# Kernel tuning notes

Measured on AMD Instinct MI355X. Metric: run time of the kernel, lower is better.

Reference implementation:

```python
import jax, jax.numpy as jnp
import numpy as np

DIM = 256
HEADS = 8
CAMS = 6
MINSIZE = 25  # AdaptiveAvgPool2d output size = min(feature_map_size)


def layernorm(x, g, b, eps=1e-5):
    mu = x.mean(-1, keepdims=True)
    var = ((x - mu) ** 2).mean(-1, keepdims=True)
    return (x - mu) / jnp.sqrt(var + eps) * g + b


def setup_inputs() -> dict:
    key = jax.random.key(0)
    ks = jax.random.split(key, 16)
    d, n = DIM, CAMS
    s = 0.02
    inp = {}
    inp["q"] = jax.random.normal(ks[0], (2, n, d, 50, 50), jnp.float32)
    inp["k"] = jax.random.normal(ks[1], (2, n, d, 50, 50), jnp.float32)
    inp["v"] = jax.random.normal(ks[2], (2, n, d, 50, 50), jnp.float32)
    inp["Wq"] = jax.random.normal(ks[3], (d, d), jnp.float32) * s
    inp["bq"] = jnp.zeros((d,), jnp.float32)
    inp["Wk"] = jax.random.normal(ks[4], (d, d), jnp.float32) * s
    inp["bk"] = jnp.zeros((d,), jnp.float32)
    inp["Wv"] = jax.random.normal(ks[5], (d, d), jnp.float32) * s
    inp["bv"] = jnp.zeros((d,), jnp.float32)
    inp["Wproj"] = jax.random.normal(ks[6], (n * d, d), jnp.float32) * s
    inp["bproj"] = jnp.zeros((d,), jnp.float32)
    inp["Waddq"] = jax.random.normal(ks[7], (n * d, d), jnp.float32) * s
    inp["baddq"] = jnp.zeros((d,), jnp.float32)
    inp["W1"] = jax.random.normal(ks[8], (d, 2 * d), jnp.float32) * s
    inp["b1"] = jnp.zeros((2 * d,), jnp.float32)
    inp["W2"] = jax.random.normal(ks[9], (2 * d, d), jnp.float32) * s
    inp["b2"] = jnp.zeros((d,), jnp.float32)
    inp["g_pre"] = jnp.ones((n * d,), jnp.float32)
    inp["b_pre"] = jnp.zeros((n * d,), jnp.float32)
    inp["g_norm"] = jnp.ones((d,), jnp.float32)
    inp["b_norm"] = jnp.zeros((d,), jnp.float32)
    return inp


def reference(q, k, v, Wq, bq, Wk, bk, Wv, bv, Wproj, bproj, Waddq, baddq,
              W1, b1, W2, b2, g_pre, b_pre, g_norm, b_norm):
    B, n, d, H, W = q.shape
    m = HEADS
    dh = d // m
    Q = H * W

    # residual query path: (b n d H W) -> (b HW (n d)) -> add_qproj -> (b HW d)
    add_q = jnp.transpose(q, (0, 3, 4, 1, 2)).reshape(B, Q, n * d) @ Waddq + baddq

    # queries: (b n d H W) -> (b n HW d) -> to_q
    qf = jnp.transpose(q, (0, 1, 3, 4, 2)).reshape(B, n, Q, d) @ Wq + bq

    # adaptive avg pool to MINSIZE (exact 2x2 bins since 50 = 2*25)
    def pool(t):
        _, _, _, h, w = t.shape
        return t.reshape(B, n, d, MINSIZE, h // MINSIZE, MINSIZE, w // MINSIZE).mean((4, 6))

    kp = pool(k)  # (b n d 25 25)
    vp = pool(v)
    K = MINSIZE * MINSIZE
    # (avg pool commutes with the pointwise linear to_k/to_v)
    kf = jnp.transpose(kp, (0, 1, 3, 4, 2)).reshape(B, n, K, d) @ Wk + bk
    vf = jnp.transpose(vp, (0, 1, 3, 4, 2)).reshape(B, n, K, d) @ Wv + bv

    # split heads
    qh = qf.reshape(B, n, Q, m, dh)
    kh = kf.reshape(B, n, K, m, dh)
    vh = vf.reshape(B, n, K, m, dh)

    # per-camera scores, softmax jointly over concatenated camera keys
    scores = (dh ** -0.5) * jnp.einsum('bnqmd,bnkmd->bmqnk', qh, kh)  # (B,m,Q,n,K)
    attn = jax.nn.softmax(scores.reshape(B, m, Q, n * K), axis=-1).reshape(B, m, Q, n, K)

    # per-camera attention output, concat cams (and heads within each cam) -> (B,Q,n*d)
    out = jnp.einsum('bmqnk,bnkmd->bqnmd', attn, vh).reshape(B, Q, n * d)

    x = layernorm(out, g_pre, b_pre) @ Wproj + bproj  # (B,Q,d)
    x = x + add_q
    h1 = jax.nn.gelu(x @ W1 + b1, approximate=False)
    x = x + layernorm(h1 @ W2 + b2, g_norm, b_norm)
    return jnp.transpose(x.reshape(B, H, W, d), (0, 3, 1, 2))  # (B,d,H,W)
```

## Files before the change

### kernel.cpp

```cpp
#include <hip/hip_runtime.h>
#include <math.h>

#define BATCH 2
#define NCAM 6
#define DIM 256
#define HEADS 8
#define DH 32
#define HW 2500
#define KP 625
#define NDIM (NCAM*DIM)

typedef __attribute__((ext_vector_type(8))) short short8;
typedef __attribute__((ext_vector_type(4))) float f32x4;

__device__ __forceinline__ short f2bf(float f) {
    union { float f; unsigned u; } v; v.f = f;
    unsigned r = v.u + 0x7fffu + ((v.u >> 16) & 1u);
    return (short)(r >> 16);
}
__device__ __forceinline__ float bf2f(short h) {
    union { unsigned u; float f; } v; v.u = ((unsigned)(unsigned short)h) << 16;
    return v.f;
}

struct WJ { const float* src; short* dst; int K, N; };
struct WArgs { WJ j[7]; };

__global__ __launch_bounds__(256) void prep_all(
    const float* __restrict__ q, const float* __restrict__ k,
    const float* __restrict__ v, short* __restrict__ qbf,
    short* __restrict__ kpbf, short* __restrict__ vpbf, WArgs wa)
{
    __shared__ float t[32][33];
    const int tx = threadIdx.x & 31, ty = threadIdx.x >> 5;
    int i = blockIdx.x;
    if (i < 7584) {
        int slab = i / 632, rem = i % 632;
        int hwB = (rem % 79) * 32, dB = (rem / 79) * 32;
        const float* src = q + (size_t)slab * 640000;
#pragma unroll
        for (int ii = 0; ii < 32; ii += 8) {
            int hw = hwB + tx;
            t[ty + ii][tx] = (hw < HW) ? src[(size_t)(dB + ty + ii) * HW + hw] : 0.f;
        }
        __syncthreads();
#pragma unroll
        for (int ii = 0; ii < 32; ii += 8) {
            int hw = hwB + ty + ii;
            if (hw < HW)
                qbf[((size_t)slab * HW + hw) * DIM + dB + tx] = f2bf(t[tx][ty + ii]);
        }
    } else if (i < 11424) {
        int i2 = i - 7584;
        const float* base; short* dst;
        if (i2 < 1920) { base = k; dst = kpbf; }
        else           { base = v; dst = vpbf; i2 -= 1920; }
        int slab = i2 / 160, rem = i2 % 160;
        int kpB = (rem % 20) * 32, dB = (rem / 20) * 32;
        const float* src = base + (size_t)slab * 640000;
        dst += (size_t)slab * (KP * DIM);
#pragma unroll
        for (int ii = 0; ii < 32; ii += 8) {
            int kp = kpB + tx;
            float val = 0.f;
            if (kp < KP) {
                int r2 = (kp / 25) * 2, c2 = (kp % 25) * 2;
                const float* p0 = src + (size_t)(dB + ty + ii) * HW + r2 * 50 + c2;
                val = 0.25f * (p0[0] + p0[1] + p0[50] + p0[51]);
            }
            t[ty + ii][tx] = val;
        }
        __syncthreads();
#pragma unroll
        for (int ii = 0; ii < 32; ii += 8) {
            int kp = kpB + ty + ii;
            if (kp < KP)
                dst[(size_t)kp * DIM + dB + tx] = f2bf(t[tx][ty + ii]);
        }
    } else {
        int wi = i - 11424;
        WJ jb = wa.j[0];
        for (int jj = 0; jj < 7; jj++) {
            jb = wa.j[jj];
            int cnt = (jb.K >> 5) * (jb.N >> 5);
            if (wi < cnt) break;
            wi -= cnt;
        }
        int tn = jb.N >> 5;
        int nB = (wi % tn) * 32, kB = (wi / tn) * 32;
#pragma unroll
        for (int ii = 0; ii < 32; ii += 8)
            t[ty + ii][tx] = jb.src[(size_t)(kB + ty + ii) * jb.N + nB + tx];
        __syncthreads();
#pragma unroll
        for (int ii = 0; ii < 32; ii += 8)
            jb.dst[(size_t)(nB + ty + ii) * jb.K + kB + tx] = f2bf(t[tx][ty + ii]);
    }
}

struct GJob { const short* A; const short* Bt; const float* bias;
              short* Cb; float* Cf; int M, K, yb, mode; };
struct GArgs { GJob j[4]; };

__global__ __launch_bounds__(256) void gemm_in(GArgs ga) {
    GJob jb = ga.j[blockIdx.z];
    if ((int)blockIdx.y >= jb.yb) return;
    __shared__ short As[64 * 32];
    __shared__ short Bs[64 * 32];

    const int tid  = threadIdx.x;
    const int nB   = blockIdx.x * 64;
    const int rB   = blockIdx.y * 64;
    const int w    = tid >> 6;
    const int lane = tid & 63;
    const int l15  = lane & 15;
    const int quad = lane >> 4;
    const int M = jb.M, K = jb.K;

    f32x4 acc[4];
#pragma unroll
    for (int jt = 0; jt < 4; jt++) acc[jt] = (f32x4){0.f, 0.f, 0.f, 0.f};

    const int r = tid >> 2, gk = tid & 3;
    const int rg = rB + r;
    const int bb = rg / 2500, hwp = rg % 2500;

    for (int kB = 0; kB < K; kB += 32) {
        __syncthreads();
        short8 a0 = {0, 0, 0, 0, 0, 0, 0, 0};
        if (rg < M) {
            if (jb.mode) {
                int kk = kB + gk * 8;
                int cam = kk >> 8, c = kk & 255;
                a0 = *(const short8*)&jb.A[(((size_t)(bb * 6 + cam)) * HW + hwp) * DIM + c];
            } else {
                a0 = *(const short8*)&jb.A[(size_t)rg * K + kB + gk * 8];
            }
        }
        *(short8*)&As[r * 32 + ((gk ^ (r & 3)) << 3)] = a0;
        short8 bv = *(const short8*)&jb.Bt[(size_t)(nB + r) * K + kB + gk * 8];
        *(short8*)&Bs[r * 32 + ((gk ^ (r & 3)) << 3)] = bv;
        __syncthreads();
        int m = w * 16 + l15;
        short8 af = *(const short8*)&As[m * 32 + ((quad ^ (m & 3)) << 3)];
#pragma unroll
        for (int jt = 0; jt < 4; jt++) {
            int n = jt * 16 + l15;
            short8 bfr = *(const short8*)&Bs[n * 32 + ((quad ^ (n & 3)) << 3)];
            acc[jt] = __builtin_amdgcn_mfma_f32_16x16x32_bf16(af, bfr, acc[jt], 0, 0, 0);
        }
    }
    int rbase = rB + w * 16 + quad * 4;
#pragma unroll
    for (int jt = 0; jt < 4; jt++) {
        int col = nB + jt * 16 + l15;
        float bcol = jb.bias[col];
#pragma unroll
        for (int reg = 0; reg < 4; reg++) {
            int rr = rbase + reg;
            if (rr < M) {
                float vv = acc[jt][reg] + bcol;
                if (jb.Cb) jb.Cb[(size_t)rr * 256 + col] = f2bf(vv);
                else       jb.Cf[(size_t)rr * 256 + col] = vv;
            }
        }
    }
}

template<int EPI, int WF32, int WBF>
__global__ __launch_bounds__(256) void mgemm_bf(
    const short* __restrict__ A, const short* __restrict__ Bt,
    const float* __restrict__ bias, const float* __restrict__ res,
    float* __restrict__ C, short* __restrict__ C2, int M, int N, int K)
{
    __shared__ short As[64 * 32];
    __shared__ short Bs[64 * 32];

    const int tid  = threadIdx.x;
    const int nB   = blockIdx.x * 64;
    const int rB   = blockIdx.y * 64;
    const int w    = tid >> 6;
    const int lane = tid & 63;
    const int l15  = lane & 15;
    const int quad = lane >> 4;

    f32x4 acc[4];
#pragma unroll
    for (int jt = 0; jt < 4; jt++) acc[jt] = (f32x4){0.f, 0.f, 0.f, 0.f};

    const int r = tid >> 2, gk = tid & 3;
    const int rg = rB + r;

    for (int kB = 0; kB < K; kB += 32) {
        __syncthreads();
        short8 a0 = {0, 0, 0, 0, 0, 0, 0, 0};
        if (rg < M) a0 = *(const short8*)&A[(size_t)rg * K + kB + gk * 8];
        *(short8*)&As[r * 32 + ((gk ^ (r & 3)) << 3)] = a0;
        short8 bv = *(const short8*)&Bt[(size_t)(nB + r) * K + kB + gk * 8];
        *(short8*)&Bs[r * 32 + ((gk ^ (r & 3)) << 3)] = bv;
        __syncthreads();
        int m = w * 16 + l15;
        short8 af = *(const short8*)&As[m * 32 + ((quad ^ (m & 3)) << 3)];
#pragma unroll
        for (int jt = 0; jt < 4; jt++) {
            int n = jt * 16 + l15;
            short8 bfr = *(const short8*)&Bs[n * 32 + ((quad ^ (n & 3)) << 3)];
            acc[jt] = __builtin_amdgcn_mfma_f32_16x16x32_bf16(af, bfr, acc[jt], 0, 0, 0);
        }
    }
    int rbase = rB + w * 16 + quad * 4;
#pragma unroll
    for (int jt = 0; jt < 4; jt++) {
        int col = nB + jt * 16 + l15;
        float bcol = bias[col];
#pragma unroll
        for (int reg = 0; reg < 4; reg++) {
            int rr = rbase + reg;
            if (rr < M) {
                float vv = acc[jt][reg] + bcol;
                if (EPI == 1) vv = 0.5f * vv * (1.f + erff(vv * 0.70710678118654752f));
                if (EPI == 2) vv += res[(size_t)rr * N + col];
                if (WF32) C[(size_t)rr * N + col] = vv;
                if (WBF)  C2[(size_t)rr * N + col] = f2bf(vv);
            }
        }
    }
}

#define TQA 64
#define CH 64
#define VSTR 72

__global__ __launch_bounds__(256) void attn_mfma(
    const short* __restrict__ qf, const short* __restrict__ kf,
    const short* __restrict__ vf, float* __restrict__ attn_out,
    float* __restrict__ Zp)
{
    const int qt  = blockIdx.x;
    const int bm  = blockIdx.y;
    const int cam = blockIdx.z;
    const int b = bm >> 3, m = bm & 7;
    const int q0 = qt * TQA;
    const int tid = threadIdx.x;
    const int w = tid >> 6, lane = tid & 63;
    const int l15 = lane & 15, quad = lane >> 4;

    __shared__ __align__(16) short Ks[CH][DH];
    __shared__ __align__(16) short Vt[DH][VSTR];
    __shared__ __align__(16) short Pl[TQA][VSTR];

    const size_t slab = (size_t)(b * 6 + cam);

    int qrow = q0 + w * 16 + l15;
    int qcl  = qrow < HW ? qrow : HW - 1;
    const short8 aq = *(const short8*)&qf[(slab * HW + qcl) * DIM + m * DH + quad * 8];

    const short* kb = kf + slab * KP * DIM + m * DH;
    const short* vb = vf + slab * KP * DIM + m * DH;

    f32x4 oacc[2];
    oacc[0] = (f32x4){0.f, 0.f, 0.f, 0.f};
    oacc[1] = (f32x4){0.f, 0.f, 0.f, 0.f};
    float zp[4] = {0.f, 0.f, 0.f, 0.f};
    const float scale = 0.17677669529663687f;

    const int kl = tid >> 2, d8 = (tid & 3) * 8;
    const int vcol = (((kl >> 3) ^ (d8 >> 3)) << 3) | (kl & 7);

    for (int c0 = 0; c0 < KP; c0 += CH) {
        __syncthreads();
        {
            int key = c0 + kl;
            short8 kv8 = {0, 0, 0, 0, 0, 0, 0, 0};
            short8 vv8 = {0, 0, 0, 0, 0, 0, 0, 0};
            if (key < KP) {
                kv8 = *(const short8*)&kb[(size_t)key * DIM + d8];
                vv8 = *(const short8*)&vb[(size_t)key * DIM + d8];
            }
            *(short8*)&Ks[kl][d8] = kv8;
#pragma unroll
            for (int t = 0; t < 8; t++) Vt[d8 + t][vcol] = vv8[t];
        }
        __syncthreads();
        f32x4 sfrag[4];
#pragma unroll
        for (int jt = 0; jt < 4; jt++) {
            short8 bk8 = *(const short8*)&Ks[jt * 16 + l15][quad * 8];
            sfrag[jt] = __builtin_amdgcn_mfma_f32_16x16x32_bf16(
                aq, bk8, (f32x4){0.f, 0.f, 0.f, 0.f}, 0, 0, 0);
        }
#pragma unroll
        for (int jt = 0; jt < 4; jt++) {
            bool valid = (c0 + jt * 16 + l15) < KP;
#pragma unroll
            for (int reg = 0; reg < 4; reg++) {
                float p = valid ? __expf(scale * sfrag[jt][reg]) : 0.f;
                short ph = f2bf(p);
                zp[reg] += bf2f(ph);
                Pl[w * 16 + quad * 4 + reg][jt * 16 + l15] = ph;
            }
        }
#pragma unroll
        for (int ks = 0; ks < 2; ks++) {
            short8 ap = *(const short8*)&Pl[w * 16 + l15][ks * 32 + quad * 8];
#pragma unroll
            for (int nt = 0; nt < 2; nt++) {
                int dhn = nt * 16 + l15;
                int pgrp = ((ks * 4 + quad) ^ (dhn >> 3));
                short8 bv8 = *(const short8*)&Vt[dhn][pgrp << 3];
                oacc[nt] = __builtin_amdgcn_mfma_f32_16x16x32_bf16(
                    ap, bv8, oacc[nt], 0, 0, 0);
            }
        }
    }
#pragma unroll
    for (int off = 1; off < 16; off <<= 1)
#pragma unroll
        for (int reg = 0; reg < 4; reg++)
            zp[reg] += __shfl_xor(zp[reg], off, 64);
#pragma unroll
    for (int reg = 0; reg < 4; reg++) {
        int q = q0 + w * 16 + quad * 4 + reg;
        if (q < HW) {
            size_t rowb = ((size_t)b * HW + q) * NDIM + cam * DIM + m * DH;
            attn_out[rowb + l15]      = oacc[0][reg];
            attn_out[rowb + 16 + l15] = oacc[1][reg];
            if (l15 == 0)
                Zp[((size_t)bm * 6 + cam) * HW + q] = zp[reg];
        }
    }
}

__global__ __launch_bounds__(256) void ln_pre_kernel(
    const float* __restrict__ xin, short* __restrict__ lnbf,
    const float* __restrict__ Zp,
    const float* __restrict__ g, const float* __restrict__ bt)
{
    const int row = blockIdx.x;
    const int tid = threadIdx.x;
    const int b = row / 2500, q = row % 2500;
    __shared__ float zinv[8];
    if (tid < 8) {
        float z = 0.f;
#pragma unroll
        for (int cam = 0; cam < 6; cam++)
            z += Zp[((size_t)(b * 8 + tid) * 6 + cam) * HW + q];
        zinv[tid] = 1.f / z;
    }
    __syncthreads();
    const float* p = xin + (size_t)row * NDIM;
    float v[6];
    float s = 0.f, ss = 0.f;
#pragma unroll
    for (int i = 0; i < 6; i++) {
        int c = tid + i * 256;
        v[i] = p[c] * zinv[(c >> 5) & 7];
        s += v[i]; ss += v[i] * v[i];
    }
    __shared__ float rs[4], rss[4];
    int lane = tid & 63, wid = tid >> 6;
#pragma unroll
    for (int o = 32; o > 0; o >>= 1) { s += __shfl_down(s, o); ss += __shfl_down(ss, o); }
    if (lane == 0) { rs[wid] = s; rss[wid] = ss; }
    __syncthreads();
    s = rs[0] + rs[1] + rs[2] + rs[3];
    ss = rss[0] + rss[1] + rss[2] + rss[3];
    float mu = s * (1.f / NDIM);
    float var = ss * (1.f / NDIM) - mu * mu;
    float inv = rsqrtf(var + 1e-5f);
#pragma unroll
    for (int i = 0; i < 6; i++) {
        int c = tid + i * 256;
        lnbf[(size_t)row * NDIM + c] = f2bf((v[i] - mu) * inv * g[c] + bt[c]);
    }
}

__global__ __launch_bounds__(256) void final_kernel2(
    const float* __restrict__ x, const float* __restrict__ y2,
    const float* __restrict__ g, const float* __restrict__ bt,
    float* __restrict__ out)
{
    __shared__ float T[256][33];
    __shared__ float ps[32][8], pss[32][8];
    __shared__ float mu_s[32], inv_s[32];
    const int tid = threadIdx.x;
    const int rl = tid & 31, seg = tid >> 5;
    const int r0 = blockIdx.x * 32;
    const int row = r0 + rl;
    const bool ok = row < 5000;

    float4 yv[8];
    float s = 0.f, ss = 0.f;
    if (ok) {
        const float4* yp = (const float4*)(y2 + (size_t)row * DIM + seg * 32);
#pragma unroll
        for (int j = 0; j < 8; j++) {
            yv[j] = yp[j];
            s += yv[j].x + yv[j].y + yv[j].z + yv[j].w;
            ss += yv[j].x * yv[j].x + yv[j].y * yv[j].y
                + yv[j].z * yv[j].z + yv[j].w * yv[j].w;
        }
    } else {
#pragma unroll
        for (int j = 0; j < 8; j++) yv[j] = (float4){0, 0, 0, 0};
    }
    ps[rl][seg] = s; pss[rl][seg] = ss;
    __syncthreads();
    if (tid < 32) {
        float a = 0.f, b2 = 0.f;
#pragma unroll
        for (int j = 0; j < 8; j++) { a += ps[tid][j]; b2 += pss[tid][j]; }
        float mu = a * (1.f / DIM);
        float var = b2 * (1.f / DIM) - mu * mu;
        mu_s[tid] = mu;
        inv_s[tid] = rsqrtf(var + 1e-5f);
    }
    __syncthreads();
    if (ok) {
        float mu = mu_s[rl], inv = inv_s[rl];
        const float4* xp = (const float4*)(x + (size_t)row * DIM + seg * 32);
#pragma unroll
        for (int j = 0; j < 8; j++) {
            float4 xv = xp[j];
            int c = seg * 32 + j * 4;
            T[c + 0][rl] = xv.x + (yv[j].x - mu) * inv * g[c + 0] + bt[c + 0];
            T[c + 1][rl] = xv.y + (yv[j].y - mu) * inv * g[c + 1] + bt[c + 1];
            T[c + 2][rl] = xv.z + (yv[j].z - mu) * inv * g[c + 2] + bt[c + 2];
            T[c + 3][rl] = xv.w + (yv[j].w - mu) * inv * g[c + 3] + bt[c + 3];
        }
    }
    __syncthreads();
    const int w = tid >> 6, lane = tid & 63;
    const int hl = lane & 31, ch = lane >> 5;
    const int rr = r0 + hl;
    if (rr < 5000) {
        int b = rr / 2500, hw = rr % 2500;
        size_t obase = (size_t)b * 640000 + hw;
#pragma unroll
        for (int it = 0; it < 32; it++) {
            int c = it * 8 + w * 2 + ch;
            out[obase + (size_t)c * 2500] = T[c][hl];
        }
    }
}

extern "C" void kernel_launch(void* const* d_in, const int* in_sizes, int n_in,
                              void* d_out, int out_size, void* d_ws, size_t ws_size,
                              hipStream_t stream)
{
    const float* q     = (const float*)d_in[0];
    const float* k     = (const float*)d_in[1];
    const float* v     = (const float*)d_in[2];
    const float* Wq    = (const float*)d_in[3];
    const float* bq    = (const float*)d_in[4];
    const float* Wk    = (const float*)d_in[5];
    const float* bk    = (const float*)d_in[6];
    const float* Wv    = (const float*)d_in[7];
    const float* bv    = (const float*)d_in[8];
    const float* Wproj = (const float*)d_in[9];
    const float* bproj = (const float*)d_in[10];
    const float* Waddq = (const float*)d_in[11];
    const float* baddq = (const float*)d_in[12];
    const float* W1    = (const float*)d_in[13];
    const float* b1    = (const float*)d_in[14];
    const float* W2    = (const float*)d_in[15];
    const float* b2    = (const float*)d_in[16];
    const float* g_pre = (const float*)d_in[17];
    const float* b_pre = (const float*)d_in[18];
    const float* g_nrm = (const float*)d_in[19];
    const float* b_nrm = (const float*)d_in[20];
    float* out = (float*)d_out;

    float* ws = (float*)d_ws;
    short* qf_a   = (short*)(ws);
    short* lnbf   = (short*)(ws);
    short* qbf    = (short*)(ws + 3840000);
    short* kf_a   = (short*)(ws + 7680000);
    short* kpbf   = (short*)(ws + 8640000);
    short* vf_a   = (short*)(ws + 9600000);
    short* vpbf   = (short*)(ws + 10560000);
    float* add_q  = ws + 11520000;
    float* attn_o = ws + 12800000;
    short* xbf    = (short*)(ws + 12800000);
    short* h1bf   = (short*)(ws + 13440000);
    float* x      = ws + 20480000;
    float* Zp     = ws + 21760000;
    short* eW     = (short*)(ws + 22000000);
    short* Wq_t    = eW;
    short* Wk_t    = eW + 65536;
    short* Wv_t    = eW + 131072;
    short* Waddq_t = eW + 196608;
    short* lW     = (short*)(ws + 22295000);
    short* Wproj_t = lW;
    short* W1_t    = lW + 393216;
    short* W2_t    = lW + 524288;
    float* y2     = ws + 22625000;

    dim3 blk(256);

    {
        WArgs wa;
        wa.j[0] = {Wq,    Wq_t,    256,  256};
        wa.j[1] = {Wk,    Wk_t,    256,  256};
        wa.j[2] = {Wv,    Wv_t,    256,  256};
        wa.j[3] = {Waddq, Waddq_t, 1536, 256};
        wa.j[4] = {Wproj, Wproj_t, 1536, 256};
        wa.j[5] = {W1,    W1_t,    256,  512};
        wa.j[6] = {W2,    W2_t,    512,  256};
        prep_all<<<dim3(12640), blk, 0, stream>>>(q, k, v, qbf, kpbf, vpbf, wa);
    }
    {
        GArgs ga;
        ga.j[0] = {qbf,  Wq_t,    bq,    qf_a, nullptr, 30000, 256,  469, 0};
        ga.j[1] = {kpbf, Wk_t,    bk,    kf_a, nullptr, 7500,  256,  118, 0};
        ga.j[2] = {vpbf, Wv_t,    bv,    vf_a, nullptr, 7500,  256,  118, 0};
        ga.j[3] = {qbf,  Waddq_t, baddq, nullptr, add_q, 5000, 1536, 79,  1};
        gemm_in<<<dim3(4, 469, 4), blk, 0, stream>>>(ga);
    }
    attn_mfma<<<dim3(40, 16, 6), blk, 0, stream>>>(qf_a, kf_a, vf_a, attn_o, Zp);
    ln_pre_kernel<<<dim3(5000), blk, 0, stream>>>(attn_o, lnbf, Zp, g_pre, b_pre);
    mgemm_bf<2, 1, 1><<<dim3(4, 79), blk, 0, stream>>>(
        lnbf, Wproj_t, bproj, add_q, x, xbf, 5000, 256, 1536);
    mgemm_bf<1, 0, 1><<<dim3(8, 79), blk, 0, stream>>>(
        xbf, W1_t, b1, nullptr, nullptr, h1bf, 5000, 512, 256);
    mgemm_bf<0, 1, 0><<<dim3(4, 79), blk, 0, stream>>>(
        h1bf, W2_t, b2, nullptr, y2, nullptr, 5000, 256, 512);
    final_kernel2<<<dim3(157), blk, 0, stream>>>(x, y2, g_nrm, b_nrm, out);
}
```

Measured before the change: 349.8 us.

## Use 128-row GEMM tiles with register prefetch and bf16 attention output

Both GEMM kernels move from 64x64 to 128x64 tiles, so each wave computes two 16-row strips and reuses the B fragments across them. The next K-slice is prefetched into registers while the current one is consumed, to hide global load latency. The attention output is stored as bf16 instead of fp32, which halves the traffic into the pre-layernorm kernel. The trade-offs are fewer blocks (lower occupancy on small M), more registers per thread, and some precision loss in the attention output.

```diff
diff --git a/kernel.cpp b/kernel.cpp
--- a/kernel.cpp
+++ b/kernel.cpp
@@ -105,63 +105,99 @@
 __global__ __launch_bounds__(256) void gemm_in(GArgs ga) {
     GJob jb = ga.j[blockIdx.z];
     if ((int)blockIdx.y >= jb.yb) return;
-    __shared__ short As[64 * 32];
+    __shared__ short As[128 * 32];
     __shared__ short Bs[64 * 32];
 
     const int tid  = threadIdx.x;
     const int nB   = blockIdx.x * 64;
-    const int rB   = blockIdx.y * 64;
+    const int rB   = blockIdx.y * 128;
     const int w    = tid >> 6;
     const int lane = tid & 63;
     const int l15  = lane & 15;
     const int quad = lane >> 4;
     const int M = jb.M, K = jb.K;
 
-    f32x4 acc[4];
-#pragma unroll
-    for (int jt = 0; jt < 4; jt++) acc[jt] = (f32x4){0.f, 0.f, 0.f, 0.f};
-
-    const int r = tid >> 2, gk = tid & 3;
-    const int rg = rB + r;
-    const int bb = rg / 2500, hwp = rg % 2500;
+    f32x4 acc[2][4];
+#pragma unroll
+    for (int i = 0; i < 2; i++)
+#pragma unroll
+        for (int jt = 0; jt < 4; jt++) acc[i][jt] = (f32x4){0.f, 0.f, 0.f, 0.f};
+
+    const int ra = tid >> 1, k0 = (tid & 1) * 16;
+    const int rga = rB + ra;
+    const int bb = rga / 2500, hwp = rga % 2500;
+    const int nb_ = tid >> 2, gkb = tid & 3;
+
+    short8 pa0 = {0,0,0,0,0,0,0,0}, pa1 = pa0, pb = pa0;
+    if (rga < M) {
+        if (jb.mode) {
+            int cam = k0 >> 8, c = k0 & 255;
+            const short* p = &jb.A[(((size_t)(bb * 6 + cam)) * HW + hwp) * DIM + c];
+            pa0 = *(const short8*)p; pa1 = *(const short8*)(p + 8);
+        } else {
+            const short* p = &jb.A[(size_t)rga * K + k0];
+            pa0 = *(const short8*)p; pa1 = *(const short8*)(p + 8);
+        }
+    }
+    pb = *(const short8*)&jb.Bt[(size_t)(nB + nb_) * K + gkb * 8];
 
     for (int kB = 0; kB < K; kB += 32) {
         __syncthreads();
-        short8 a0 = {0, 0, 0, 0, 0, 0, 0, 0};
-        if (rg < M) {
-            if (jb.mode) {
-                int kk = kB + gk * 8;
-                int cam = kk >> 8, c = kk & 255;
-                a0 = *(const short8*)&jb.A[(((size_t)(bb * 6 + cam)) * HW + hwp) * DIM + c];
-            } else {
-                a0 = *(const short8*)&jb.A[(size_t)rg * K + kB + gk * 8];
-            }
-        }
-        *(short8*)&As[r * 32 + ((gk ^ (r & 3)) << 3)] = a0;
-        short8 bv = *(const short8*)&jb.Bt[(size_t)(nB + r) * K + kB + gk * 8];
-        *(short8*)&Bs[r * 32 + ((gk ^ (r & 3)) << 3)] = bv;
-        __syncthreads();
-        int m = w * 16 + l15;
-        short8 af = *(const short8*)&As[m * 32 + ((quad ^ (m & 3)) << 3)];
+        {
+            int g0 = k0 >> 3;
+            *(short8*)&As[ra * 32 + ((g0 ^ (ra & 3)) << 3)]       = pa0;
+            *(short8*)&As[ra * 32 + (((g0 + 1) ^ (ra & 3)) << 3)] = pa1;
+            *(short8*)&Bs[nb_ * 32 + ((gkb ^ (nb_ & 3)) << 3)]    = pb;
+        }
+        __syncthreads();
+        int kN = kB + 32;
+        if (kN < K) {
+            if (rga < M) {
+                if (jb.mode) {
+                    int kk = kN + k0;
+                    int cam = kk >> 8, c = kk & 255;
+                    const short* p = &jb.A[(((size_t)(bb * 6 + cam)) * HW + hwp) * DIM + c];
+                    pa0 = *(const short8*)p; pa1 = *(const short8*)(p + 8);
+                } else {
+                    const short* p = &jb.A[(size_t)rga * K + kN + k0];
+                    pa0 = *(const short8*)p; pa1 = *(const short8*)(p + 8);
+                }
+            }
+            pb = *(const short8*)&jb.Bt[(size_t)(nB + nb_) * K + kN + gkb * 8];
+        }
+        short8 af[2], bfr[4];
+#pragma unroll
+        for (int i = 0; i < 2; i++) {
+            int m = w * 32 + i * 16 + l15;
+            af[i] = *(const short8*)&As[m * 32 + ((quad ^ (m & 3)) << 3)];
+        }
 #pragma unroll
         for (int jt = 0; jt < 4; jt++) {
             int n = jt * 16 + l15;
-            short8 bfr = *(const short8*)&Bs[n * 32 + ((quad ^ (n & 3)) << 3)];
-            acc[jt] = __builtin_amdgcn_mfma_f32_16x16x32_bf16(af, bfr, acc[jt], 0, 0, 0);
-        }
-    }
-    int rbase = rB + w * 16 + quad * 4;
-#pragma unroll
-    for (int jt = 0; jt < 4; jt++) {
-        int col = nB + jt * 16 + l15;
-        float bcol = jb.bias[col];
-#pragma unroll
-        for (int reg = 0; reg < 4; reg++) {
-            int rr = rbase + reg;
-            if (rr < M) {
-                float vv = acc[jt][reg] + bcol;
-                if (jb.Cb) jb.Cb[(size_t)rr * 256 + col] = f2bf(vv);
-                else       jb.Cf[(size_t)rr * 256 + col] = vv;
+            bfr[jt] = *(const short8*)&Bs[n * 32 + ((quad ^ (n & 3)) << 3)];
+        }
+#pragma unroll
+        for (int i = 0; i < 2; i++)
+#pragma unroll
+            for (int jt = 0; jt < 4; jt++)
+                acc[i][jt] = __builtin_amdgcn_mfma_f32_16x16x32_bf16(
+                    af[i], bfr[jt], acc[i][jt], 0, 0, 0);
+    }
+#pragma unroll
+    for (int i = 0; i < 2; i++) {
+        int rbase = rB + w * 32 + i * 16 + quad * 4;
+#pragma unroll
+        for (int jt = 0; jt < 4; jt++) {
+            int col = nB + jt * 16 + l15;
+            float bcol = jb.bias[col];
+#pragma unroll
+            for (int reg = 0; reg < 4; reg++) {
+                int rr = rbase + reg;
+                if (rr < M) {
+                    float vv = acc[i][jt][reg] + bcol;
+                    if (jb.Cb) jb.Cb[(size_t)rr * 256 + col] = f2bf(vv);
+                    else       jb.Cf[(size_t)rr * 256 + col] = vv;
+                }
             }
         }
     }
@@ -173,55 +209,86 @@
     const float* __restrict__ bias, const float* __restrict__ res,
     float* __restrict__ C, short* __restrict__ C2, int M, int N, int K)
 {
-    __shared__ short As[64 * 32];
+    __shared__ short As[128 * 32];
     __shared__ short Bs[64 * 32];
 
     const int tid  = threadIdx.x;
     const int nB   = blockIdx.x * 64;
-    const int rB   = blockIdx.y * 64;
+    const int rB   = blockIdx.y * 128;
     const int w    = tid >> 6;
     const int lane = tid & 63;
     const int l15  = lane & 15;
     const int quad = lane >> 4;
 
-    f32x4 acc[4];
-#pragma unroll
-    for (int jt = 0; jt < 4; jt++) acc[jt] = (f32x4){0.f, 0.f, 0.f, 0.f};
-
-    const int r = tid >> 2, gk = tid & 3;
-    const int rg = rB + r;
+    f32x4 acc[2][4];
+#pragma unroll
+    for (int i = 0; i < 2; i++)
+#pragma unroll
+        for (int jt = 0; jt < 4; jt++) acc[i][jt] = (f32x4){0.f, 0.f, 0.f, 0.f};
+
+    const int ra = tid >> 1, k0 = (tid & 1) * 16;
+    const int rga = rB + ra;
+    const int nb_ = tid >> 2, gkb = tid & 3;
+
+    short8 pa0 = {0,0,0,0,0,0,0,0}, pa1 = pa0, pb = pa0;
+    if (rga < M) {
+        const short* p = &A[(size_t)rga * K + k0];
+        pa0 = *(const short8*)p; pa1 = *(const short8*)(p + 8);
+    }
+    pb = *(const short8*)&Bt[(size_t)(nB + nb_) * K + gkb * 8];
 
     for (int kB = 0; kB < K; kB += 32) {
         __syncthreads();
-        short8 a0 = {0, 0, 0, 0, 0, 0, 0, 0};
-        if (rg < M) a0 = *(const short8*)&A[(size_t)rg * K + kB + gk * 8];
-        *(short8*)&As[r * 32 + ((gk ^ (r & 3)) << 3)] = a0;
-        short8 bv = *(const short8*)&Bt[(size_t)(nB + r) * K + kB + gk * 8];
-        *(short8*)&Bs[r * 32 + ((gk ^ (r & 3)) << 3)] = bv;
-        __syncthreads();
-        int m = w * 16 + l15;
-        short8 af = *(const short8*)&As[m * 32 + ((quad ^ (m & 3)) << 3)];
+        {
+            int g0 = k0 >> 3;
+            *(short8*)&As[ra * 32 + ((g0 ^ (ra & 3)) << 3)]       = pa0;
+            *(short8*)&As[ra * 32 + (((g0 + 1) ^ (ra & 3)) << 3)] = pa1;
+            *(short8*)&Bs[nb_ * 32 + ((gkb ^ (nb_ & 3)) << 3)]    = pb;
+        }
+        __syncthreads();
+        int kN = kB + 32;
+        if (kN < K) {
+            if (rga < M) {
+                const short* p = &A[(size_t)rga * K + kN + k0];
+                pa0 = *(const short8*)p; pa1 = *(const short8*)(p + 8);
+            }
+            pb = *(const short8*)&Bt[(size_t)(nB + nb_) * K + kN + gkb * 8];
+        }
+        short8 af[2], bfr[4];
+#pragma unroll
+        for (int i = 0; i < 2; i++) {
+            int m = w * 32 + i * 16 + l15;
+            af[i] = *(const short8*)&As[m * 32 + ((quad ^ (m & 3)) << 3)];
+        }
 #pragma unroll
         for (int jt = 0; jt < 4; jt++) {
             int n = jt * 16 + l15;
-            short8 bfr = *(const short8*)&Bs[n * 32 + ((quad ^ (n & 3)) << 3)];
-            acc[jt] = __builtin_amdgcn_mfma_f32_16x16x32_bf16(af, bfr, acc[jt], 0, 0, 0);
-        }
-    }
-    int rbase = rB + w * 16 + quad * 4;
-#pragma unroll
-    for (int jt = 0; jt < 4; jt++) {
-        int col = nB + jt * 16 + l15;
-        float bcol = bias[col];
-#pragma unroll
-        for (int reg = 0; reg < 4; reg++) {
-            int rr = rbase + reg;
-            if (rr < M) {
-                float vv = acc[jt][reg] + bcol;
-                if (EPI == 1) vv = 0.5f * vv * (1.f + erff(vv * 0.70710678118654752f));
-                if (EPI == 2) vv += res[(size_t)rr * N + col];
-                if (WF32) C[(size_t)rr * N + col] = vv;
-                if (WBF)  C2[(size_t)rr * N + col] = f2bf(vv);
+            bfr[jt] = *(const short8*)&Bs[n * 32 + ((quad ^ (n & 3)) << 3)];
+        }
+#pragma unroll
+        for (int i = 0; i < 2; i++)
+#pragma unroll
+            for (int jt = 0; jt < 4; jt++)
+                acc[i][jt] = __builtin_amdgcn_mfma_f32_16x16x32_bf16(
+                    af[i], bfr[jt], acc[i][jt], 0, 0, 0);
+    }
+#pragma unroll
+    for (int i = 0; i < 2; i++) {
+        int rbase = rB + w * 32 + i * 16 + quad * 4;
+#pragma unroll
+        for (int jt = 0; jt < 4; jt++) {
+            int col = nB + jt * 16 + l15;
+            float bcol = bias[col];
+#pragma unroll
+            for (int reg = 0; reg < 4; reg++) {
+                int rr = rbase + reg;
+                if (rr < M) {
+                    float vv = acc[i][jt][reg] + bcol;
+                    if (EPI == 1) vv = 0.5f * vv * (1.f + erff(vv * 0.70710678118654752f));
+                    if (EPI == 2) vv += res[(size_t)rr * N + col];
+                    if (WF32) C[(size_t)rr * N + col] = vv;
+                    if (WBF)  C2[(size_t)rr * N + col] = f2bf(vv);
+                }
             }
         }
     }
@@ -233,7 +300,7 @@
 
 __global__ __launch_bounds__(256) void attn_mfma(
     const short* __restrict__ qf, const short* __restrict__ kf,
-    const short* __restrict__ vf, float* __restrict__ attn_out,
+    const short* __restrict__ vf, short* __restrict__ attn_out,
     float* __restrict__ Zp)
 {
     const int qt  = blockIdx.x;
@@ -323,8 +390,8 @@
         int q = q0 + w * 16 + quad * 4 + reg;
         if (q < HW) {
             size_t rowb = ((size_t)b * HW + q) * NDIM + cam * DIM + m * DH;
-            attn_out[rowb + l15]      = oacc[0][reg];
-            attn_out[rowb + 16 + l15] = oacc[1][reg];
+            attn_out[rowb + l15]      = f2bf(oacc[0][reg]);
+            attn_out[rowb + 16 + l15] = f2bf(oacc[1][reg]);
             if (l15 == 0)
                 Zp[((size_t)bm * 6 + cam) * HW + q] = zp[reg];
         }
@@ -332,7 +399,7 @@
 }
 
 __global__ __launch_bounds__(256) void ln_pre_kernel(
-    const float* __restrict__ xin, short* __restrict__ lnbf,
+    const short* __restrict__ xin, short* __restrict__ lnbf,
     const float* __restrict__ Zp,
     const float* __restrict__ g, const float* __restrict__ bt)
 {
@@ -348,13 +415,13 @@
         zinv[tid] = 1.f / z;
     }
     __syncthreads();
-    const float* p = xin + (size_t)row * NDIM;
+    const short* p = xin + (size_t)row * NDIM;
     float v[6];
     float s = 0.f, ss = 0.f;
 #pragma unroll
     for (int i = 0; i < 6; i++) {
         int c = tid + i * 256;
-        v[i] = p[c] * zinv[(c >> 5) & 7];
+        v[i] = bf2f(p[c]) * zinv[(c >> 5) & 7];
         s += v[i]; ss += v[i] * v[i];
     }
     __shared__ float rs[4], rss[4];
@@ -480,7 +547,7 @@
     short* vf_a   = (short*)(ws + 9600000);
     short* vpbf   = (short*)(ws + 10560000);
     float* add_q  = ws + 11520000;
-    float* attn_o = ws + 12800000;
+    short* attn_o = (short*)(ws + 12800000);
     short* xbf    = (short*)(ws + 12800000);
     short* h1bf   = (short*)(ws + 13440000);
     float* x      = ws + 20480000;
@@ -511,19 +578,19 @@
     }
     {
         GArgs ga;
-        ga.j[0] = {qbf,  Wq_t,    bq,    qf_a, nullptr, 30000, 256,  469, 0};
-        ga.j[1] = {kpbf, Wk_t,    bk,    kf_a, nullptr, 7500,  256,  118, 0};
-        ga.j[2] = {vpbf, Wv_t,    bv,    vf_a, nullptr, 7500,  256,  118, 0};
-        ga.j[3] = {qbf,  Waddq_t, baddq, nullptr, add_q, 5000, 1536, 79,  1};
-        gemm_in<<<dim3(4, 469, 4), blk, 0, stream>>>(ga);
+        ga.j[0] = {qbf,  Wq_t,    bq,    qf_a, nullptr, 30000, 256,  235, 0};
+        ga.j[1] = {kpbf, Wk_t,    bk,    kf_a, nullptr, 7500,  256,  59,  0};
+        ga.j[2] = {vpbf, Wv_t,    bv,    vf_a, nullptr, 7500,  256,  59,  0};
+        ga.j[3] = {qbf,  Waddq_t, baddq, nullptr, add_q, 5000, 1536, 40,  1};
+        gemm_in<<<dim3(4, 235, 4), blk, 0, stream>>>(ga);
     }
     attn_mfma<<<dim3(40, 16, 6), blk, 0, stream>>>(qf_a, kf_a, vf_a, attn_o, Zp);
     ln_pre_kernel<<<dim3(5000), blk, 0, stream>>>(attn_o, lnbf, Zp, g_pre, b_pre);
-    mgemm_bf<2, 1, 1><<<dim3(4, 79), blk, 0, stream>>>(
+    mgemm_bf<2, 1, 1><<<dim3(4, 40), blk, 0, stream>>>(
         lnbf, Wproj_t, bproj, add_q, x, xbf, 5000, 256, 1536);
-    mgemm_bf<1, 0, 1><<<dim3(8, 79), blk, 0, stream>>>(
+    mgemm_bf<1, 0, 1><<<dim3(8, 40), blk, 0, stream>>>(
         xbf, W1_t, b1, nullptr, nullptr, h1bf, 5000, 512, 256);
-    mgemm_bf<0, 1, 0><<<dim3(4, 79), blk, 0, stream>>>(
+    mgemm_bf<0, 1, 0><<<dim3(4, 40), blk, 0, stream>>>(
         h1bf, W2_t, b2, nullptr, y2, nullptr, 5000, 256, 512);
     final_kernel2<<<dim3(157), blk, 0, stream>>>(x, y2, g_nrm, b_nrm, out);
 }
```

Result: faster. 342.8 us (-2.0%).
